# Kernel optimization log

Hardware: AMD Instinct MI355X
Metric: run time of the kernel (lower is better)

Reference implementation:

```python
import jax, jax.numpy as jnp
import numpy as np

B, DIM, K, NH = 65536, 8, 64, 100
TOTAL = DIM * K


def setup_inputs() -> dict:
    key = jax.random.key(0)
    ks = jax.random.split(key, 14)
    e = jax.random.normal(ks[0], (B, DIM, K), dtype=jnp.float32)
    # strictly upper-triangular DAG adjacency: C[j, i] = 1 iff j < i (j is a parent of i)
    C = jnp.triu(jnp.ones((DIM, DIM), dtype=jnp.int32), k=1)
    sc = 0.05
    inp = {"e": e, "C": C}
    inp["sW1"] = jax.random.normal(ks[1], (TOTAL, NH), dtype=jnp.float32) * sc
    inp["sb1"] = jnp.zeros((NH,), dtype=jnp.float32)
    inp["sW2"] = jax.random.normal(ks[2], (NH, NH), dtype=jnp.float32) * sc
    inp["sb2"] = jnp.zeros((NH,), dtype=jnp.float32)
    inp["sW3"] = jax.random.normal(ks[3], (NH, K), dtype=jnp.float32) * sc
    inp["sb3"] = jnp.zeros((K,), dtype=jnp.float32)
    inp["tW1"] = jax.random.normal(ks[4], (TOTAL, NH), dtype=jnp.float32) * sc
    inp["tb1"] = jnp.zeros((NH,), dtype=jnp.float32)
    inp["tW2"] = jax.random.normal(ks[5], (NH, NH), dtype=jnp.float32) * sc
    inp["tb2"] = jnp.zeros((NH,), dtype=jnp.float32)
    inp["tW3"] = jax.random.normal(ks[6], (NH, K), dtype=jnp.float32) * sc
    inp["tb3"] = jnp.zeros((K,), dtype=jnp.float32)
    return inp


def _mlp(x, mask, W1, b1, W2, b2, W3, b3):
    # MLP.forward: net(x * mask); Linear->ReLU->Linear->ReLU->Linear->Sigmoid
    h = jax.nn.relu((x * mask) @ W1 + b1)
    h = jax.nn.relu(h @ W2 + b2)
    return jax.nn.sigmoid(h @ W3 + b3)


def reference(e, C, sW1, sb1, sW2, sb2, sW3, sb3, tW1, tb1, tW2, tb2, tW3, tb3):
    b, dim, k = e.shape
    total = dim * k
    # mask for step i: column C[:, i] with each entry repeated k times -> [total]
    # (if column i is all zeros, mask is zeros, matching the elif branch)
    masks = jnp.repeat(C.astype(e.dtype), k, axis=0).T  # [dim, total]
    e_steps = jnp.swapaxes(e, 0, 1)  # [dim, B, k]

    def step(z, xs):
        i, mask, e_i = xs
        zf = z.reshape(b, total)
        s = _mlp(zf, mask, sW1, sb1, sW2, sb2, sW3, sb3)  # [B, k]
        t = _mlp(zf, mask, tW1, tb1, tW2, tb2, tW3, tb3)  # [B, k]
        z = z.at[:, i, :].set(jnp.exp(s) * e_i + t)
        return z, jnp.sum(s, axis=1)

    z0 = jnp.zeros_like(e)
    z, ld_steps = jax.lax.scan(step, z0, (jnp.arange(dim), masks, e_steps))
    log_det = jnp.sum(ld_steps, axis=0)  # [B]
    return z, log_det
```

## Files before the change

### kernel.cpp

```cpp
#include <hip/hip_runtime.h>

#define B_SZ 65536
#define NH   100

typedef __bf16 bf16_t;
typedef __bf16 bf16x2 __attribute__((ext_vector_type(2)));
typedef __bf16 bf16x8 __attribute__((ext_vector_type(8)));
typedef float  f32x4  __attribute__((ext_vector_type(4)));
typedef unsigned u32x2 __attribute__((ext_vector_type(2)));

#define SZ_W2 14336
#define SZ_W3 8192
#define SZ_W1 7168
#define OFF_W3   28672
#define OFF_W1   45056
#define WS_TOTAL 145408

__global__ void prep_weights(const float* __restrict__ sW1, const float* __restrict__ sW2,
                             const float* __restrict__ sW3, const float* __restrict__ tW1,
                             const float* __restrict__ tW2, const float* __restrict__ tW3,
                             bf16_t* __restrict__ ws) {
  int idx = blockIdx.x * 256 + threadIdx.x;
  if (idx >= WS_TOTAL) return;
  float v = 0.f;
  if (idx < 2 * SZ_W2) {
    const float* W = (idx < SZ_W2) ? sW2 : tW2;
    int l = (idx < SZ_W2) ? idx : idx - SZ_W2;
    int j = l & 7, ln = (l >> 3) & 63, kc = (l >> 9) & 3, mt = l >> 11;
    int k = kc * 32 + (ln >> 4) * 8 + j;
    int m = mt * 16 + (ln & 15);
    v = (k < NH && m < NH) ? W[k * NH + m] : 0.f;
  } else if (idx < OFF_W1) {
    int l = idx - OFF_W3;
    const float* W = (l < SZ_W3) ? sW3 : tW3;
    l &= (SZ_W3 - 1);
    int j = l & 7, ln = (l >> 3) & 63, kc = (l >> 9) & 3, mt = l >> 11;
    int k = kc * 32 + (ln >> 4) * 8 + j;
    int m = mt * 16 + (ln & 15);
    v = (k < NH) ? W[k * 64 + m] : 0.f;
  } else {
    int l = idx - OFF_W1;
    int b = l / (2 * SZ_W1);
    int r2 = l - b * 2 * SZ_W1;
    const float* W = (r2 < SZ_W1) ? sW1 : tW1;
    int w = (r2 < SZ_W1) ? r2 : r2 - SZ_W1;
    int j = w & 7, ln = (w >> 3) & 63, kc = (w >> 9) & 1, mt = w >> 10;
    int k = kc * 32 + (ln >> 4) * 8 + j;
    int m = mt * 16 + (ln & 15);
    v = (m < NH) ? W[(b * 64 + k) * NH + m] : 0.f;
  }
  ws[idx] = (bf16_t)v;
}

__global__ void prep_bias(const float* __restrict__ sb1, const float* __restrict__ sb2,
                          const float* __restrict__ sb3, const float* __restrict__ tb1,
                          const float* __restrict__ tb2, const float* __restrict__ tb3,
                          float* __restrict__ fb) {
  int t = threadIdx.x;
  if (t < 112)       fb[t] = (t < NH) ? sb2[t] : 0.f;
  else if (t < 224)  fb[t] = (t - 112 < NH) ? tb2[t - 112] : 0.f;
  else if (t < 288)  fb[t] = sb3[t - 224];
  else if (t < 352)  fb[t] = tb3[t - 288];
  else if (t < 464)  fb[t] = (t - 352 < NH) ? sb1[t - 352] : 0.f;
  else if (t < 576)  fb[t] = (t - 464 < NH) ? tb1[t - 464] : 0.f;
}

__device__ __forceinline__ void gload_lds16(const void* gptr, void* lptr) {
  __builtin_amdgcn_global_load_lds(
      (const __attribute__((address_space(1))) unsigned int*)gptr,
      (__attribute__((address_space(3))) unsigned int*)lptr, 16, 0, 0);
}

__device__ __forceinline__ unsigned pk2(float a, float b) {
  bf16x2 t = {(bf16_t)a, (bf16_t)b};
  return __builtin_bit_cast(unsigned, t);
}

#if __has_builtin(__builtin_amdgcn_permlane32_swap) && __has_builtin(__builtin_amdgcn_permlane16_swap)
__device__ __forceinline__ void plswap(unsigned &x, unsigned &y) {
  u32x2 a = __builtin_amdgcn_permlane32_swap(x, y, false, false);
  u32x2 b = __builtin_amdgcn_permlane16_swap(a[0], a[1], false, false);
  x = b[0]; y = b[1];
}
#else
__device__ __forceinline__ void plswap(unsigned &x, unsigned &y) {
  unsigned xo, yo;
  asm volatile("v_mov_b32 %0, %2\n\t"
               "v_mov_b32 %1, %3\n\t"
               "s_nop 1\n\t"
               "v_permlane32_swap_b32 %0, %1\n\t"
               "s_nop 1\n\t"
               "v_permlane16_swap_b32 %0, %1"
               : "=&v"(xo), "=&v"(yo) : "v"(x), "v"(y));
  x = xo; y = yo;
}
#endif

__device__ __forceinline__ bf16x8 build_bfrag(unsigned lo0, unsigned lo1,
                                              unsigned hi0, unsigned hi1) {
  plswap(lo0, hi0);
  plswap(lo1, hi1);
  union { unsigned u[4]; bf16x8 v; } r;
  r.u[0] = lo0; r.u[1] = lo1; r.u[2] = hi0; r.u[3] = hi1;
  return r.v;
}

struct __align__(16) SMem {
  bf16_t w2[2 * SZ_W2];
  bf16_t w3[2 * SZ_W3];
  bf16_t w1[2][2 * SZ_W1];
  float  bias[512];
};

__global__ __launch_bounds__(512, 2) void flow_kernel(
    const float* __restrict__ e,
    const bf16_t* __restrict__ wf,
    const float* __restrict__ fb,
    float* __restrict__ out) {
  __shared__ SMem sm;

  const int tid  = threadIdx.x;
  const int wave = tid >> 6;
  const int lane = tid & 63;
  const int c    = lane & 15;
  const int Q    = lane >> 4;
  const int rowBase = blockIdx.x * 256 + wave * 32;

  {
    const char* g = (const char*)wf;
    char* l = (char*)&sm;
    const char* gb = (const char*)fb;
    #pragma unroll
    for (int t = 0; t < 15; ++t) {
      const int ch = t * 8 + wave;
      if (ch < 116)      gload_lds16(g + ch * 1024 + lane * 16, l + ch * 1024);
      else if (ch < 118) gload_lds16(gb + (ch - 116) * 1024 + lane * 16,
                                     (char*)sm.bias + (ch - 116) * 1024);
    }
  }

  f32x4 acc1S[2][7], acc1T[2][7];
  #pragma unroll
  for (int th = 0; th < 7; ++th) {
    const f32x4 vs = *(const f32x4*)(fb + 352 + th * 16 + Q * 4);
    const f32x4 vt = *(const f32x4*)(fb + 464 + th * 16 + Q * 4);
    acc1S[0][th] = vs; acc1S[1][th] = vs;
    acc1T[0][th] = vt; acc1T[1][th] = vt;
  }
  float ldacc[2] = {0.f, 0.f};

  __syncthreads();

  const float* lb2S = sm.bias;
  const float* lb2T = sm.bias + 112;
  const float* lb3S = sm.bias + 224;
  const float* lb3T = sm.bias + 288;

  auto run_net = [&](const f32x4 (&acc1)[2][7], const bf16_t* __restrict__ w2f,
                     const bf16_t* __restrict__ w3f, const float* __restrict__ lb2,
                     const float* __restrict__ lb3, f32x4 (&acc3)[2][4]) {
    unsigned pk[2][7][2];
    #pragma unroll
    for (int mt = 0; mt < 2; ++mt)
      #pragma unroll
      for (int th = 0; th < 7; ++th) {
        pk[mt][th][0] = pk2(fmaxf(acc1[mt][th][0], 0.f), fmaxf(acc1[mt][th][1], 0.f));
        pk[mt][th][1] = pk2(fmaxf(acc1[mt][th][2], 0.f), fmaxf(acc1[mt][th][3], 0.f));
      }
    f32x4 acc2[2][7];
    #pragma unroll
    for (int th = 0; th < 7; ++th) {
      const f32x4 bv = *(const f32x4*)(lb2 + th * 16 + Q * 4);
      acc2[0][th] = bv; acc2[1][th] = bv;
    }
    #pragma unroll
    for (int kc = 0; kc < 4; ++kc) {
      const int tlo = kc * 2, thi = (kc * 2 + 1 > 6) ? 5 : kc * 2 + 1;
      const bf16x8 b0 = build_bfrag(pk[0][tlo][0], pk[0][tlo][1], pk[0][thi][0], pk[0][thi][1]);
      const bf16x8 b1 = build_bfrag(pk[1][tlo][0], pk[1][tlo][1], pk[1][thi][0], pk[1][thi][1]);
      #pragma unroll
      for (int th = 0; th < 7; ++th) {
        const bf16x8 A = *(const bf16x8*)(w2f + ((th * 4 + kc) * 64 + lane) * 8);
        acc2[0][th] = __builtin_amdgcn_mfma_f32_16x16x32_bf16(A, b0, acc2[0][th], 0, 0, 0);
        acc2[1][th] = __builtin_amdgcn_mfma_f32_16x16x32_bf16(A, b1, acc2[1][th], 0, 0, 0);
      }
    }
    #pragma unroll
    for (int mt = 0; mt < 2; ++mt)
      #pragma unroll
      for (int th = 0; th < 7; ++th) {
        pk[mt][th][0] = pk2(fmaxf(acc2[mt][th][0], 0.f), fmaxf(acc2[mt][th][1], 0.f));
        pk[mt][th][1] = pk2(fmaxf(acc2[mt][th][2], 0.f), fmaxf(acc2[mt][th][3], 0.f));
      }
    #pragma unroll
    for (int ot = 0; ot < 4; ++ot) {
      const f32x4 bv = *(const f32x4*)(lb3 + ot * 16 + Q * 4);
      acc3[0][ot] = bv; acc3[1][ot] = bv;
    }
    #pragma unroll
    for (int kc = 0; kc < 4; ++kc) {
      const int tlo = kc * 2, thi = (kc * 2 + 1 > 6) ? 5 : kc * 2 + 1;
      const bf16x8 b0 = build_bfrag(pk[0][tlo][0], pk[0][tlo][1], pk[0][thi][0], pk[0][thi][1]);
      const bf16x8 b1 = build_bfrag(pk[1][tlo][0], pk[1][tlo][1], pk[1][thi][0], pk[1][thi][1]);
      #pragma unroll
      for (int ot = 0; ot < 4; ++ot) {
        const bf16x8 A = *(const bf16x8*)(w3f + ((ot * 4 + kc) * 64 + lane) * 8);
        acc3[0][ot] = __builtin_amdgcn_mfma_f32_16x16x32_bf16(A, b0, acc3[0][ot], 0, 0, 0);
        acc3[1][ot] = __builtin_amdgcn_mfma_f32_16x16x32_bf16(A, b1, acc3[1][ot], 0, 0, 0);
      }
    }
  };

  for (int i = 0; i < 8; ++i) {
    f32x4 acc3S[2][4], acc3T[2][4];
    run_net(acc1S, sm.w2,         sm.w3,         lb2S, lb3S, acc3S);
    run_net(acc1T, sm.w2 + SZ_W2, sm.w3 + SZ_W3, lb2T, lb3T, acc3T);

    unsigned zpk[2][4][2];
    #pragma unroll
    for (int mt = 0; mt < 2; ++mt) {
      #pragma unroll
      for (int ot = 0; ot < 4; ++ot) {
        const int off = (rowBase + mt * 16 + c) * 512 + i * 64 + ot * 16 + Q * 4;
        const f32x4 ev = *(const f32x4*)(e + off);
        f32x4 zv;
        float ss = 0.f;
        #pragma unroll
        for (int r = 0; r < 4; ++r) {
          const float sv = __builtin_amdgcn_rcpf(1.f + __expf(-acc3S[mt][ot][r]));
          const float tv = __builtin_amdgcn_rcpf(1.f + __expf(-acc3T[mt][ot][r]));
          zv[r] = __expf(sv) * ev[r] + tv;
          ss += sv;
        }
        __builtin_nontemporal_store(zv, (f32x4*)(out + off));
        zpk[mt][ot][0] = pk2(zv[0], zv[1]);
        zpk[mt][ot][1] = pk2(zv[2], zv[3]);
        ldacc[mt] += ss;
      }
    }

    if (i < 7) {
      __syncthreads();
      const bf16_t* __restrict__ w1b = sm.w1[i & 1];
      #pragma unroll
      for (int kc = 0; kc < 2; ++kc) {
        const bf16x8 b0 = build_bfrag(zpk[0][kc * 2][0], zpk[0][kc * 2][1],
                                      zpk[0][kc * 2 + 1][0], zpk[0][kc * 2 + 1][1]);
        const bf16x8 b1 = build_bfrag(zpk[1][kc * 2][0], zpk[1][kc * 2][1],
                                      zpk[1][kc * 2 + 1][0], zpk[1][kc * 2 + 1][1]);
        #pragma unroll
        for (int th = 0; th < 7; ++th) {
          const bf16x8 AS = *(const bf16x8*)(w1b + ((th * 2 + kc) * 64 + lane) * 8);
          const bf16x8 AT = *(const bf16x8*)(w1b + SZ_W1 + ((th * 2 + kc) * 64 + lane) * 8);
          acc1S[0][th] = __builtin_amdgcn_mfma_f32_16x16x32_bf16(AS, b0, acc1S[0][th], 0, 0, 0);
          acc1S[1][th] = __builtin_amdgcn_mfma_f32_16x16x32_bf16(AS, b1, acc1S[1][th], 0, 0, 0);
          acc1T[0][th] = __builtin_amdgcn_mfma_f32_16x16x32_bf16(AT, b0, acc1T[0][th], 0, 0, 0);
          acc1T[1][th] = __builtin_amdgcn_mfma_f32_16x16x32_bf16(AT, b1, acc1T[1][th], 0, 0, 0);
        }
      }
      if (i < 6) {
        const char* g = (const char*)wf + 90112 + (i + 1) * 28672;
        char* l = (char*)sm.w1[(i + 1) & 1];
        #pragma unroll
        for (int t = 0; t < 4; ++t) {
          const int ch = t * 8 + wave;
          if (ch < 28) gload_lds16(g + ch * 1024 + lane * 16, l + ch * 1024);
        }
      }
    }
  }

  #pragma unroll
  for (int mt = 0; mt < 2; ++mt) {
    float v = ldacc[mt];
    v += __shfl_xor(v, 16);
    v += __shfl_xor(v, 32);
    if (Q == 0) out[B_SZ * 512 + rowBase + mt * 16 + c] = v;
  }
}

extern "C" void kernel_launch(void* const* d_in, const int* in_sizes, int n_in,
                              void* d_out, int out_size, void* d_ws, size_t ws_size,
                              hipStream_t stream) {
  (void)in_sizes; (void)n_in; (void)out_size; (void)ws_size;
  const float* e   = (const float*)d_in[0];
  const float* sW1 = (const float*)d_in[2];
  const float* sb1 = (const float*)d_in[3];
  const float* sW2 = (const float*)d_in[4];
  const float* sb2 = (const float*)d_in[5];
  const float* sW3 = (const float*)d_in[6];
  const float* sb3 = (const float*)d_in[7];
  const float* tW1 = (const float*)d_in[8];
  const float* tb1 = (const float*)d_in[9];
  const float* tW2 = (const float*)d_in[10];
  const float* tb2 = (const float*)d_in[11];
  const float* tW3 = (const float*)d_in[12];
  const float* tb3 = (const float*)d_in[13];
  bf16_t* ws = (bf16_t*)d_ws;
  float*  fb = (float*)(ws + WS_TOTAL);
  float* out = (float*)d_out;

  prep_weights<<<(WS_TOTAL + 255) / 256, 256, 0, stream>>>(sW1, sW2, sW3, tW1, tW2, tW3, ws);
  prep_bias<<<1, 576, 0, stream>>>(sb1, sb2, sb3, tb1, tb2, tb3, fb);
  flow_kernel<<<256, 512, 0, stream>>>(e, ws, fb, out);
}
```

Measured before the change: 319.1 us.

## Halve rows per wave and double block size to 1024 threads

Each wave now processes 16 batch rows instead of 32, and the block grows to 16 waves covering the same 256 rows. This halves accumulator register use per wave and doubles the number of resident waves per CU, giving more latency hiding. In exchange, each LDS weight fragment feeds only one MFMA per load instead of two, doubling LDS read traffic for weights. The launch bound also changes to 1024 threads, which tightens the per-thread register budget.

```diff
diff --git a/kernel.cpp b/kernel.cpp
--- a/kernel.cpp
+++ b/kernel.cpp
@@ -112,7 +112,7 @@
   float  bias[512];
 };
 
-__global__ __launch_bounds__(512, 2) void flow_kernel(
+__global__ __launch_bounds__(1024, 4) void flow_kernel(
     const float* __restrict__ e,
     const bf16_t* __restrict__ wf,
     const float* __restrict__ fb,
@@ -124,30 +124,28 @@
   const int lane = tid & 63;
   const int c    = lane & 15;
   const int Q    = lane >> 4;
-  const int rowBase = blockIdx.x * 256 + wave * 32;
+  const int rowBase = blockIdx.x * 256 + wave * 16;
 
   {
     const char* g = (const char*)wf;
     char* l = (char*)&sm;
     const char* gb = (const char*)fb;
     #pragma unroll
-    for (int t = 0; t < 15; ++t) {
-      const int ch = t * 8 + wave;
+    for (int t = 0; t < 8; ++t) {
+      const int ch = t * 16 + wave;
       if (ch < 116)      gload_lds16(g + ch * 1024 + lane * 16, l + ch * 1024);
       else if (ch < 118) gload_lds16(gb + (ch - 116) * 1024 + lane * 16,
                                      (char*)sm.bias + (ch - 116) * 1024);
     }
   }
 
-  f32x4 acc1S[2][7], acc1T[2][7];
+  f32x4 acc1S[7], acc1T[7];
   #pragma unroll
   for (int th = 0; th < 7; ++th) {
-    const f32x4 vs = *(const f32x4*)(fb + 352 + th * 16 + Q * 4);
-    const f32x4 vt = *(const f32x4*)(fb + 464 + th * 16 + Q * 4);
-    acc1S[0][th] = vs; acc1S[1][th] = vs;
-    acc1T[0][th] = vt; acc1T[1][th] = vt;
-  }
-  float ldacc[2] = {0.f, 0.f};
+    acc1S[th] = *(const f32x4*)(fb + 352 + th * 16 + Q * 4);
+    acc1T[th] = *(const f32x4*)(fb + 464 + th * 16 + Q * 4);
+  }
+  float ldacc = 0.f;
 
   __syncthreads();
 
@@ -156,87 +154,72 @@
   const float* lb3S = sm.bias + 224;
   const float* lb3T = sm.bias + 288;
 
-  auto run_net = [&](const f32x4 (&acc1)[2][7], const bf16_t* __restrict__ w2f,
+  auto run_net = [&](const f32x4 (&acc1)[7], const bf16_t* __restrict__ w2f,
                      const bf16_t* __restrict__ w3f, const float* __restrict__ lb2,
-                     const float* __restrict__ lb3, f32x4 (&acc3)[2][4]) {
-    unsigned pk[2][7][2];
-    #pragma unroll
-    for (int mt = 0; mt < 2; ++mt)
-      #pragma unroll
-      for (int th = 0; th < 7; ++th) {
-        pk[mt][th][0] = pk2(fmaxf(acc1[mt][th][0], 0.f), fmaxf(acc1[mt][th][1], 0.f));
-        pk[mt][th][1] = pk2(fmaxf(acc1[mt][th][2], 0.f), fmaxf(acc1[mt][th][3], 0.f));
-      }
-    f32x4 acc2[2][7];
+                     const float* __restrict__ lb3, f32x4 (&acc3)[4]) {
+    unsigned pk[7][2];
     #pragma unroll
     for (int th = 0; th < 7; ++th) {
-      const f32x4 bv = *(const f32x4*)(lb2 + th * 16 + Q * 4);
-      acc2[0][th] = bv; acc2[1][th] = bv;
-    }
+      pk[th][0] = pk2(fmaxf(acc1[th][0], 0.f), fmaxf(acc1[th][1], 0.f));
+      pk[th][1] = pk2(fmaxf(acc1[th][2], 0.f), fmaxf(acc1[th][3], 0.f));
+    }
+    f32x4 acc2[7];
+    #pragma unroll
+    for (int th = 0; th < 7; ++th)
+      acc2[th] = *(const f32x4*)(lb2 + th * 16 + Q * 4);
     #pragma unroll
     for (int kc = 0; kc < 4; ++kc) {
       const int tlo = kc * 2, thi = (kc * 2 + 1 > 6) ? 5 : kc * 2 + 1;
-      const bf16x8 b0 = build_bfrag(pk[0][tlo][0], pk[0][tlo][1], pk[0][thi][0], pk[0][thi][1]);
-      const bf16x8 b1 = build_bfrag(pk[1][tlo][0], pk[1][tlo][1], pk[1][thi][0], pk[1][thi][1]);
+      const bf16x8 b0 = build_bfrag(pk[tlo][0], pk[tlo][1], pk[thi][0], pk[thi][1]);
       #pragma unroll
       for (int th = 0; th < 7; ++th) {
         const bf16x8 A = *(const bf16x8*)(w2f + ((th * 4 + kc) * 64 + lane) * 8);
-        acc2[0][th] = __builtin_amdgcn_mfma_f32_16x16x32_bf16(A, b0, acc2[0][th], 0, 0, 0);
-        acc2[1][th] = __builtin_amdgcn_mfma_f32_16x16x32_bf16(A, b1, acc2[1][th], 0, 0, 0);
-      }
-    }
-    #pragma unroll
-    for (int mt = 0; mt < 2; ++mt)
-      #pragma unroll
-      for (int th = 0; th < 7; ++th) {
-        pk[mt][th][0] = pk2(fmaxf(acc2[mt][th][0], 0.f), fmaxf(acc2[mt][th][1], 0.f));
-        pk[mt][th][1] = pk2(fmaxf(acc2[mt][th][2], 0.f), fmaxf(acc2[mt][th][3], 0.f));
-      }
-    #pragma unroll
-    for (int ot = 0; ot < 4; ++ot) {
-      const f32x4 bv = *(const f32x4*)(lb3 + ot * 16 + Q * 4);
-      acc3[0][ot] = bv; acc3[1][ot] = bv;
-    }
+        acc2[th] = __builtin_amdgcn_mfma_f32_16x16x32_bf16(A, b0, acc2[th], 0, 0, 0);
+      }
+    }
+    #pragma unroll
+    for (int th = 0; th < 7; ++th) {
+      pk[th][0] = pk2(fmaxf(acc2[th][0], 0.f), fmaxf(acc2[th][1], 0.f));
+      pk[th][1] = pk2(fmaxf(acc2[th][2], 0.f), fmaxf(acc2[th][3], 0.f));
+    }
+    #pragma unroll
+    for (int ot = 0; ot < 4; ++ot)
+      acc3[ot] = *(const f32x4*)(lb3 + ot * 16 + Q * 4);
     #pragma unroll
     for (int kc = 0; kc < 4; ++kc) {
       const int tlo = kc * 2, thi = (kc * 2 + 1 > 6) ? 5 : kc * 2 + 1;
-      const bf16x8 b0 = build_bfrag(pk[0][tlo][0], pk[0][tlo][1], pk[0][thi][0], pk[0][thi][1]);
-      const bf16x8 b1 = build_bfrag(pk[1][tlo][0], pk[1][tlo][1], pk[1][thi][0], pk[1][thi][1]);
+      const bf16x8 b0 = build_bfrag(pk[tlo][0], pk[tlo][1], pk[thi][0], pk[thi][1]);
       #pragma unroll
       for (int ot = 0; ot < 4; ++ot) {
         const bf16x8 A = *(const bf16x8*)(w3f + ((ot * 4 + kc) * 64 + lane) * 8);
-        acc3[0][ot] = __builtin_amdgcn_mfma_f32_16x16x32_bf16(A, b0, acc3[0][ot], 0, 0, 0);
-        acc3[1][ot] = __builtin_amdgcn_mfma_f32_16x16x32_bf16(A, b1, acc3[1][ot], 0, 0, 0);
+        acc3[ot] = __builtin_amdgcn_mfma_f32_16x16x32_bf16(A, b0, acc3[ot], 0, 0, 0);
       }
     }
   };
 
   for (int i = 0; i < 8; ++i) {
-    f32x4 acc3S[2][4], acc3T[2][4];
+    f32x4 acc3S[4], acc3T[4];
     run_net(acc1S, sm.w2,         sm.w3,         lb2S, lb3S, acc3S);
     run_net(acc1T, sm.w2 + SZ_W2, sm.w3 + SZ_W3, lb2T, lb3T, acc3T);
 
-    unsigned zpk[2][4][2];
-    #pragma unroll
-    for (int mt = 0; mt < 2; ++mt) {
-      #pragma unroll
-      for (int ot = 0; ot < 4; ++ot) {
-        const int off = (rowBase + mt * 16 + c) * 512 + i * 64 + ot * 16 + Q * 4;
-        const f32x4 ev = *(const f32x4*)(e + off);
-        f32x4 zv;
-        float ss = 0.f;
-        #pragma unroll
-        for (int r = 0; r < 4; ++r) {
-          const float sv = __builtin_amdgcn_rcpf(1.f + __expf(-acc3S[mt][ot][r]));
-          const float tv = __builtin_amdgcn_rcpf(1.f + __expf(-acc3T[mt][ot][r]));
-          zv[r] = __expf(sv) * ev[r] + tv;
-          ss += sv;
-        }
-        __builtin_nontemporal_store(zv, (f32x4*)(out + off));
-        zpk[mt][ot][0] = pk2(zv[0], zv[1]);
-        zpk[mt][ot][1] = pk2(zv[2], zv[3]);
-        ldacc[mt] += ss;
-      }
+    unsigned zpk[4][2];
+    #pragma unroll
+    for (int ot = 0; ot < 4; ++ot) {
+      const int off = (rowBase + c) * 512 + i * 64 + ot * 16 + Q * 4;
+      const f32x4 ev = *(const f32x4*)(e + off);
+      f32x4 zv;
+      float ss = 0.f;
+      #pragma unroll
+      for (int r = 0; r < 4; ++r) {
+        const float sv = __builtin_amdgcn_rcpf(1.f + __expf(-acc3S[ot][r]));
+        const float tv = __builtin_amdgcn_rcpf(1.f + __expf(-acc3T[ot][r]));
+        zv[r] = __expf(sv) * ev[r] + tv;
+        ss += sv;
+      }
+      __builtin_nontemporal_store(zv, (f32x4*)(out + off));
+      zpk[ot][0] = pk2(zv[0], zv[1]);
+      zpk[ot][1] = pk2(zv[2], zv[3]);
+      ldacc += ss;
     }
 
     if (i < 7) {
@@ -244,38 +227,33 @@
       const bf16_t* __restrict__ w1b = sm.w1[i & 1];
       #pragma unroll
       for (int kc = 0; kc < 2; ++kc) {
-        const bf16x8 b0 = build_bfrag(zpk[0][kc * 2][0], zpk[0][kc * 2][1],
-                                      zpk[0][kc * 2 + 1][0], zpk[0][kc * 2 + 1][1]);
-        const bf16x8 b1 = build_bfrag(zpk[1][kc * 2][0], zpk[1][kc * 2][1],
-                                      zpk[1][kc * 2 + 1][0], zpk[1][kc * 2 + 1][1]);
+        const bf16x8 b0 = build_bfrag(zpk[kc * 2][0], zpk[kc * 2][1],
+                                      zpk[kc * 2 + 1][0], zpk[kc * 2 + 1][1]);
         #pragma unroll
         for (int th = 0; th < 7; ++th) {
           const bf16x8 AS = *(const bf16x8*)(w1b + ((th * 2 + kc) * 64 + lane) * 8);
           const bf16x8 AT = *(const bf16x8*)(w1b + SZ_W1 + ((th * 2 + kc) * 64 + lane) * 8);
-          acc1S[0][th] = __builtin_amdgcn_mfma_f32_16x16x32_bf16(AS, b0, acc1S[0][th], 0, 0, 0);
-          acc1S[1][th] = __builtin_amdgcn_mfma_f32_16x16x32_bf16(AS, b1, acc1S[1][th], 0, 0, 0);
-          acc1T[0][th] = __builtin_amdgcn_mfma_f32_16x16x32_bf16(AT, b0, acc1T[0][th], 0, 0, 0);
-          acc1T[1][th] = __builtin_amdgcn_mfma_f32_16x16x32_bf16(AT, b1, acc1T[1][th], 0, 0, 0);
+          acc1S[th] = __builtin_amdgcn_mfma_f32_16x16x32_bf16(AS, b0, acc1S[th], 0, 0, 0);
+          acc1T[th] = __builtin_amdgcn_mfma_f32_16x16x32_bf16(AT, b0, acc1T[th], 0, 0, 0);
         }
       }
       if (i < 6) {
         const char* g = (const char*)wf + 90112 + (i + 1) * 28672;
         char* l = (char*)sm.w1[(i + 1) & 1];
         #pragma unroll
-        for (int t = 0; t < 4; ++t) {
-          const int ch = t * 8 + wave;
+        for (int t = 0; t < 2; ++t) {
+          const int ch = t * 16 + wave;
           if (ch < 28) gload_lds16(g + ch * 1024 + lane * 16, l + ch * 1024);
         }
       }
     }
   }
 
-  #pragma unroll
-  for (int mt = 0; mt < 2; ++mt) {
-    float v = ldacc[mt];
+  {
+    float v = ldacc;
     v += __shfl_xor(v, 16);
     v += __shfl_xor(v, 32);
-    if (Q == 0) out[B_SZ * 512 + rowBase + mt * 16 + c] = v;
+    if (Q == 0) out[B_SZ * 512 + rowBase + c] = v;
   }
 }
 
@@ -302,5 +280,5 @@
 
   prep_weights<<<(WS_TOTAL + 255) / 256, 256, 0, stream>>>(sW1, sW2, sW3, tW1, tW2, tW3, ws);
   prep_bias<<<1, 576, 0, stream>>>(sb1, sb2, sb3, tb1, tb2, tb3, fb);
-  flow_kernel<<<256, 512, 0, stream>>>(e, ws, fb, out);
-}
+  flow_kernel<<<256, 1024, 0, stream>>>(e, ws, fb, out);
+}
```

Result: slower. 335.6 us (+5.2%).
